# Kernel optimization log

Hardware: AMD Instinct MI355X
Metric: run time of the kernel (lower is better)

Reference implementation:

```python
import jax, jax.numpy as jnp
import numpy as np

IN_SIZE = 32
NUM_ACTIONS = 90
ACTION_DIM = 32
INNER_DIM = 256
HIDDEN_DIM = 512
N_LAYERS = 2
WORLD_STATE_SIZE = 32
# last 8 features are categorical (binary) flags, first 24 numeric
CAT_FLAGS = np.zeros(WORLD_STATE_SIZE, dtype=bool)
CAT_FLAGS[24:] = True


def setup_inputs() -> dict:
    key = jax.random.key(0)
    ks = jax.random.split(key, 20)
    s = 0.05
    b, t = 64, 512
    inp = {
        "batch_world_states_tensor": jax.random.normal(ks[0], (b, t, IN_SIZE), jnp.float32),
        "batch_action_indices": jax.random.randint(ks[1], (b, t), 0, NUM_ACTIONS),
        "action_emb": jax.random.normal(ks[2], (NUM_ACTIONS, ACTION_DIM), jnp.float32),
        "in_w": jax.random.normal(ks[3], (INNER_DIM - ACTION_DIM, IN_SIZE), jnp.float32) * s,
        "in_b": jax.random.normal(ks[4], (INNER_DIM - ACTION_DIM,), jnp.float32) * 0.005,
        "w_ih0": jax.random.normal(ks[5], (4 * HIDDEN_DIM, INNER_DIM), jnp.float32) * s,
        "w_hh0": jax.random.normal(ks[6], (4 * HIDDEN_DIM, HIDDEN_DIM), jnp.float32) * s,
        "b_ih0": jax.random.normal(ks[7], (4 * HIDDEN_DIM,), jnp.float32) * 0.005,
        "b_hh0": jax.random.normal(ks[8], (4 * HIDDEN_DIM,), jnp.float32) * 0.005,
        "w_ih1": jax.random.normal(ks[9], (4 * HIDDEN_DIM, HIDDEN_DIM), jnp.float32) * s,
        "w_hh1": jax.random.normal(ks[10], (4 * HIDDEN_DIM, HIDDEN_DIM), jnp.float32) * s,
        "b_ih1": jax.random.normal(ks[11], (4 * HIDDEN_DIM,), jnp.float32) * 0.005,
        "b_hh1": jax.random.normal(ks[12], (4 * HIDDEN_DIM,), jnp.float32) * 0.005,
        "out_w1": jax.random.normal(ks[13], (2 * HIDDEN_DIM, HIDDEN_DIM), jnp.float32) * s,
        "out_b1": jax.random.normal(ks[14], (2 * HIDDEN_DIM,), jnp.float32) * 0.005,
        "out_w2": jax.random.normal(ks[15], (WORLD_STATE_SIZE, 2 * HIDDEN_DIM), jnp.float32) * s,
        "out_b2": jax.random.normal(ks[16], (WORLD_STATE_SIZE,), jnp.float32) * 0.005,
    }
    return inp


def _lstm_layer(x, w_ih, w_hh, b_ih, b_hh):
    """x: [b, s, d_in] -> ([b, s, H], h_T, c_T). PyTorch gate order i,f,g,o."""
    b = x.shape[0]
    H = w_hh.shape[1]
    # precompute input-to-hidden contributions for all steps: [s, b, 4H]
    gx = jnp.einsum('bsd,gd->sbg', x, w_ih) + b_ih + b_hh
    h0 = jnp.zeros((b, H), x.dtype)
    c0 = jnp.zeros((b, H), x.dtype)

    def step(carry, g_t):
        h, c = carry
        g = g_t + h @ w_hh.T  # [b, 4H]
        i, f, gg, o = jnp.split(g, 4, axis=-1)
        i = jax.nn.sigmoid(i)
        f = jax.nn.sigmoid(f)
        gg = jnp.tanh(gg)
        o = jax.nn.sigmoid(o)
        c = f * c + i * gg
        h = o * jnp.tanh(c)
        return (h, c), h

    (hT, cT), hs = jax.lax.scan(step, (h0, c0), gx)
    return hs.transpose(1, 0, 2), hT, cT  # [b, s, H]


def reference(batch_world_states_tensor, batch_action_indices, action_emb,
              in_w, in_b, w_ih0, w_hh0, b_ih0, b_hh0,
              w_ih1, w_hh1, b_ih1, b_hh1,
              out_w1, out_b1, out_w2, out_b2):
    # input projection + action embedding concat
    proj = jax.nn.relu(jnp.einsum('bsd,ed->bse', batch_world_states_tensor, in_w) + in_b)
    acts = action_emb[batch_action_indices]  # [b, s, action_dim]
    x = jnp.concatenate([proj, acts], axis=-1)  # [b, s, inner_dim]
    # 2-layer LSTM
    x, h0T, c0T = _lstm_layer(x, w_ih0, w_hh0, b_ih0, b_hh0)
    rnn_out, h1T, c1T = _lstm_layer(x, w_ih1, w_hh1, b_ih1, b_hh1)
    # out projector
    hmid = jax.nn.relu(jnp.einsum('bsh,eh->bse', rnn_out, out_w1) + out_b1)
    out = jnp.einsum('bse,de->bsd', hmid, out_w2) + out_b2  # [b, s, D]
    # sigmoid on categorical feature slots
    cat_mask = jnp.asarray(CAT_FLAGS)
    out = jnp.where(cat_mask, jax.nn.sigmoid(out), out)
    return out[:, -1, :]  # [b, D]
```

## Files before the change

### kernel.cpp

```cpp
#include <hip/hip_runtime.h>

#define T_STEPS 512
#define BATCH   64
#define IN_SZ   32
#define AD      32
#define INNER   256
#define PROJ    224
#define HID     512
#define SENTW   0x7F7F7F7Fu
#define SENT64  0x7F7F7F7F7F7F7F7FULL
#define DEP     16
#define RST     6
#define SLOTW   4096

typedef __attribute__((ext_vector_type(8))) short short8;
typedef __attribute__((ext_vector_type(4))) float f32x4;

static __device__ __forceinline__ unsigned short f2bf(float f) {
  unsigned int u = __float_as_uint(f);
  u += 0x7FFFu + ((u >> 16) & 1u);
  return (unsigned short)(u >> 16);
}
static __device__ __forceinline__ float sigmoidf_(float x) { return 1.f / (1.f + __expf(-x)); }
static __device__ __forceinline__ float tanhf_(float x) {
  float e = __expf(-2.f * fabsf(x));
  float r = (1.f - e) / (1.f + e);
  return x < 0.f ? -r : r;
}

__global__ __launch_bounds__(256) void k_prep(
    const float* __restrict__ ws_in, const int* __restrict__ act_idx,
    const float* __restrict__ emb, const float* __restrict__ in_w,
    const float* __restrict__ in_b, unsigned short* __restrict__ x_bf)
{
  int t = blockIdx.x;
  int tid = threadIdx.x;
  __shared__ float st[BATCH * IN_SZ];
  __shared__ int ai[BATCH];
  for (int i = tid; i < BATCH * IN_SZ; i += 256) {
    int b = i >> 5, k = i & 31;
    st[i] = ws_in[((size_t)b * T_STEPS + t) * IN_SZ + k];
  }
  if (tid < BATCH) ai[tid] = act_idx[tid * T_STEPS + t];
  __syncthreads();
  if (tid < PROJ) {
    float w[IN_SZ];
    const float* wrow = in_w + tid * IN_SZ;
#pragma unroll
    for (int k = 0; k < IN_SZ; ++k) w[k] = wrow[k];
    float bb = in_b[tid];
    for (int b = 0; b < BATCH; ++b) {
      float acc = bb;
      const float* sb = st + b * IN_SZ;
#pragma unroll
      for (int k = 0; k < IN_SZ; ++k) acc += w[k] * sb[k];
      x_bf[((size_t)t * BATCH + b) * INNER + tid] = f2bf(fmaxf(acc, 0.f));
    }
  } else {
    int j = tid - PROJ;
    for (int b = 0; b < BATCH; ++b)
      x_bf[((size_t)t * BATCH + b) * INNER + tid] = f2bf(emb[ai[b] * AD + j]);
  }
}

static __device__ __forceinline__ short8 bfrag_load(const float* __restrict__ w, int stride, int row, int k0) {
  const float* p = w + (size_t)row * stride + k0;
  f32x4 a = *reinterpret_cast<const f32x4*>(p);
  f32x4 b = *reinterpret_cast<const f32x4*>(p + 4);
  short8 r;
  r[0] = (short)f2bf(a[0]); r[1] = (short)f2bf(a[1]); r[2] = (short)f2bf(a[2]); r[3] = (short)f2bf(a[3]);
  r[4] = (short)f2bf(b[0]); r[5] = (short)f2bf(b[1]); r[6] = (short)f2bf(b[2]); r[7] = (short)f2bf(b[3]);
  return r;
}

struct Frag64 { unsigned long long u[8]; };
union FU2 { unsigned long long u[2]; short8 s; };

static __device__ __forceinline__ void ld64(const unsigned long long* q, Frag64& f) {
#pragma unroll
  for (int kk = 0; kk < 4; ++kk) {
    f.u[kk * 2]     = __hip_atomic_load(q + kk * 128,     __ATOMIC_RELAXED, __HIP_MEMORY_SCOPE_AGENT);
    f.u[kk * 2 + 1] = __hip_atomic_load(q + kk * 128 + 1, __ATOMIC_RELAXED, __HIP_MEMORY_SCOPE_AGENT);
  }
}
static __device__ __forceinline__ bool fragok(const Frag64& f) {
  bool ok = true;
#pragma unroll
  for (int i = 0; i < 8; ++i)
    ok = ok & ((unsigned)(f.u[i] >> 32) != SENTW) & ((unsigned)f.u[i] != SENTW);
  return ok;
}
static __device__ __forceinline__ Frag64 poll_one(const unsigned long long* q) {
  Frag64 f;
  int miss = 0;
  while (true) {
    ld64(q, f);
    if (__all((int)fragok(f))) break;
    if (++miss > 2) __builtin_amdgcn_s_sleep(1);
  }
  return f;
}
static __device__ __forceinline__ void poll_two(const unsigned long long* qa, const unsigned long long* qb,
                                                Frag64& fa, Frag64& fb) {
  int miss = 0;
  while (true) {
    ld64(qa, fa);
    ld64(qb, fb);
    if (__all((int)(fragok(fa) & fragok(fb)))) break;
    if (++miss > 2) __builtin_amdgcn_s_sleep(1);
  }
}

static __device__ __forceinline__ void mfma4(const Frag64& f, const short8* wf, f32x4* acc) {
#pragma unroll
  for (int kk = 0; kk < 4; ++kk) {
    FU2 u; u.u[0] = f.u[kk * 2]; u.u[1] = f.u[kk * 2 + 1];
#pragma unroll
    for (int g = 0; g < 4; ++g)
      acc[g] = __builtin_amdgcn_mfma_f32_16x16x32_bf16(u.s, wf[g * 4 + kk], acc[g], 0, 0, 0);
  }
}

static __device__ __forceinline__ void st_agent(unsigned int* p, unsigned int v) {
  __hip_atomic_store(p, v, __ATOMIC_RELAXED, __HIP_MEMORY_SCOPE_AGENT);
}
static __device__ __forceinline__ void st_agent64(unsigned long long* p, unsigned long long v) {
  __hip_atomic_store(p, v, __ATOMIC_RELAXED, __HIP_MEMORY_SCOPE_AGENT);
}
static __device__ __forceinline__ size_t slotw(int bg, int d) { return ((size_t)(bg * DEP + d)) * SLOTW; }

template<int L>
static __device__ void lstm_body(
    const unsigned short* __restrict__ x_bf,
    const float* __restrict__ wih, const float* __restrict__ whh,
    const float* __restrict__ bih, const float* __restrict__ bhh,
    unsigned int* __restrict__ h0w, unsigned int* __restrict__ h1w,
    float* __restrict__ h1fin, unsigned int* __restrict__ flags,
    int bg, int blk, float* __restrict__ spart)
{
  constexpr int KI = (L == 0) ? 2 : 4;

  const int tid  = threadIdx.x;
  const int lane = tid & 63;
  const int wv   = tid >> 6;
  const int q    = lane >> 4;
  const int ln   = lane & 15;
  const int hid0 = blk << 4;
  const int m    = tid >> 4;
  const int n    = tid & 15;
  const int cb64 = (wv * 8 + (q >> 1)) * 64 + ln * 4 + (q & 1) * 2;

  float bias[4];
#pragma unroll
  for (int g = 0; g < 4; ++g)
    bias[g] = bih[g * HID + hid0 + n] + bhh[g * HID + hid0 + n];

  short8 fih[4 * KI];
#pragma unroll
  for (int g = 0; g < 4; ++g)
#pragma unroll
    for (int kk = 0; kk < KI; ++kk)
      fih[g * KI + kk] = bfrag_load(wih, (L == 0) ? INNER : HID,
                                    g * HID + hid0 + ln, (wv * KI + kk) * 32 + q * 8);
  short8 fhh[16];
#pragma unroll
  for (int g = 0; g < 4; ++g)
#pragma unroll
    for (int kk = 0; kk < 4; ++kk)
      fhh[g * 4 + kk] = bfrag_load(whh, HID, g * HID + hid0 + ln, (wv * 4 + kk) * 32 + q * 8);

  const int wo64 = blk * 64 + m * 4 + (n >> 2);
  float c_state = 0.f;

  for (int t = 0; t < T_STEPS; ++t) {
    f32x4 acc[4];
#pragma unroll
    for (int g = 0; g < 4; ++g) acc[g] = (f32x4){0.f, 0.f, 0.f, 0.f};

    if constexpr (L == 0) {
      const unsigned long long* hq = reinterpret_cast<const unsigned long long*>(
          h0w + slotw(bg, (t - 1) & (DEP - 1))) + cb64;
      Frag64 f0;
      if (t > 0) ld64(hq, f0);

      const unsigned short* xr = x_bf + ((size_t)t * BATCH + bg * 16 + ln) * INNER + q * 8;
#pragma unroll
      for (int kk = 0; kk < KI; ++kk) {
        short8 xa = *reinterpret_cast<const short8*>(xr + (wv * KI + kk) * 32);
#pragma unroll
        for (int g = 0; g < 4; ++g)
          acc[g] = __builtin_amdgcn_mfma_f32_16x16x32_bf16(xa, fih[g * KI + kk], acc[g], 0, 0, 0);
      }
      if ((t & 3) == 0 && t >= 8) {
        const unsigned int* fp = flags + (bg * 32 + (lane & 31)) * 32;
        unsigned int tgt = (unsigned)(t - 4);
        while (true) {
          unsigned int v = __hip_atomic_load(fp, __ATOMIC_RELAXED, __HIP_MEMORY_SCOPE_AGENT);
          if (__all((int)(v >= tgt))) break;
          __builtin_amdgcn_s_sleep(1);
        }
        asm volatile("" ::: "memory");
      }
      if (t > 0) {
        if (!__all((int)fragok(f0))) f0 = poll_one(hq);
        mfma4(f0, fhh, acc);
      }
    } else {
      if (t > 0) {
        Frag64 fa, fb;
        poll_two(reinterpret_cast<const unsigned long long*>(h1w + slotw(bg, (t - 1) & (DEP - 1))) + cb64,
                 reinterpret_cast<const unsigned long long*>(h0w + slotw(bg, t & (DEP - 1))) + cb64, fa, fb);
        mfma4(fa, fhh, acc);
        mfma4(fb, fih, acc);
      } else {
        Frag64 fb = poll_one(reinterpret_cast<const unsigned long long*>(h0w + slotw(bg, 0)) + cb64);
        mfma4(fb, fih, acc);
      }
    }

    float* sp_w = spart + (t & 1) * 4096;
#pragma unroll
    for (int g = 0; g < 4; ++g)
      *reinterpret_cast<f32x4*>(sp_w + ((((wv * 4 + g) * 4 + q) * 16 + ln) * 4)) = acc[g];
    __syncthreads();

    if constexpr (L == 1) {
      if ((t & 1) == 1 && tid == 0)
        st_agent(flags + (bg * 32 + blk) * 32, (unsigned)(t + 1));
    }

    float gate[4];
#pragma unroll
    for (int g = 0; g < 4; ++g) {
      float s = bias[g];
#pragma unroll
      for (int w2 = 0; w2 < 4; ++w2)
        s += sp_w[(((w2 * 4 + g) * 4 + (m >> 2)) * 16 + n) * 4 + (m & 3)];
      gate[g] = s;
    }
    float gi = sigmoidf_(gate[0]);
    float gf = sigmoidf_(gate[1]);
    float gc = tanhf_(gate[2]);
    float go = sigmoidf_(gate[3]);
    c_state = gf * c_state + gi * gc;
    float h = go * tanhf_(c_state);

    float hp = __shfl_xor(h, 1);
    unsigned int wword = (unsigned)f2bf(h) | ((unsigned)f2bf(hp) << 16);
    unsigned int wy = __shfl_down(wword, 2);
    unsigned long long dw = (unsigned long long)wword | ((unsigned long long)wy << 32);
    if constexpr (L == 0) {
      if (!(n & 3)) {
        st_agent64(reinterpret_cast<unsigned long long*>(h0w + slotw(bg, t & (DEP - 1))) + wo64, dw);
        st_agent64(reinterpret_cast<unsigned long long*>(h0w + slotw(bg, (t + RST) & (DEP - 1))) + wo64, SENT64);
      }
    } else {
      if (!(n & 3)) {
        st_agent64(reinterpret_cast<unsigned long long*>(h1w + slotw(bg, t & (DEP - 1))) + wo64, dw);
        st_agent64(reinterpret_cast<unsigned long long*>(h1w + slotw(bg, (t + RST) & (DEP - 1))) + wo64, SENT64);
      }
      if (t == T_STEPS - 1)
        h1fin[(size_t)(bg * 16 + m) * HID + hid0 + n] = h;
    }
  }
}

__global__ __launch_bounds__(256, 1) void k_lstm(
    const unsigned short* __restrict__ x_bf,
    const float* __restrict__ w_ih0, const float* __restrict__ w_hh0,
    const float* __restrict__ b_ih0, const float* __restrict__ b_hh0,
    const float* __restrict__ w_ih1, const float* __restrict__ w_hh1,
    const float* __restrict__ b_ih1, const float* __restrict__ b_hh1,
    unsigned int* h0w, unsigned int* h1w, float* h1fin, unsigned int* flags)
{
  __shared__ float spart[2 * 4096];
  const int xg  = blockIdx.x & 7;
  const int blk = blockIdx.x >> 3;
  const int bg  = xg & 3;
  if (xg < 4)
    lstm_body<0>(x_bf, w_ih0, w_hh0, b_ih0, b_hh0, h0w, h1w, h1fin, flags, bg, blk, spart);
  else
    lstm_body<1>(x_bf, w_ih1, w_hh1, b_ih1, b_hh1, h0w, h1w, h1fin, flags, bg, blk, spart);
}

__global__ __launch_bounds__(256) void k_head(
    const float* __restrict__ h1, const float* __restrict__ w1, const float* __restrict__ b1,
    const float* __restrict__ w2, const float* __restrict__ b2, float* __restrict__ out)
{
  int b = blockIdx.x, tid = threadIdx.x;
  __shared__ float sh[HID];
  __shared__ float sm[2 * HID];
  for (int k = tid; k < HID; k += 256) sh[k] = h1[(size_t)b * HID + k];
  __syncthreads();
#pragma unroll
  for (int r0 = 0; r0 < 4; ++r0) {
    int row = r0 * 256 + tid;
    const f32x4* wr = reinterpret_cast<const f32x4*>(w1 + (size_t)row * HID);
    float s = 0.f;
#pragma unroll 4
    for (int k = 0; k < HID / 4; ++k) {
      f32x4 v = wr[k];
      s += v[0] * sh[k * 4] + v[1] * sh[k * 4 + 1] + v[2] * sh[k * 4 + 2] + v[3] * sh[k * 4 + 3];
    }
    sm[row] = fmaxf(b1[row] + s, 0.f);
  }
  __syncthreads();
  if (tid < 32) {
    const f32x4* wr = reinterpret_cast<const f32x4*>(w2 + (size_t)tid * 2 * HID);
    float s = b2[tid];
#pragma unroll 4
    for (int k = 0; k < 2 * HID / 4; ++k) {
      f32x4 v = wr[k];
      s += v[0] * sm[k * 4] + v[1] * sm[k * 4 + 1] + v[2] * sm[k * 4 + 2] + v[3] * sm[k * 4 + 3];
    }
    if (tid >= 24) s = sigmoidf_(s);
    out[b * 32 + tid] = s;
  }
}

extern "C" void kernel_launch(void* const* d_in, const int* in_sizes, int n_in,
                              void* d_out, int out_size, void* d_ws, size_t ws_size,
                              hipStream_t stream) {
  const float* ws_in  = (const float*)d_in[0];
  const int*   aidx   = (const int*)d_in[1];
  const float* emb    = (const float*)d_in[2];
  const float* in_w   = (const float*)d_in[3];
  const float* in_b   = (const float*)d_in[4];
  const float* w_ih0  = (const float*)d_in[5];
  const float* w_hh0  = (const float*)d_in[6];
  const float* b_ih0  = (const float*)d_in[7];
  const float* b_hh0  = (const float*)d_in[8];
  const float* w_ih1  = (const float*)d_in[9];
  const float* w_hh1  = (const float*)d_in[10];
  const float* b_ih1  = (const float*)d_in[11];
  const float* b_hh1  = (const float*)d_in[12];
  const float* out_w1 = (const float*)d_in[13];
  const float* out_b1 = (const float*)d_in[14];
  const float* out_w2 = (const float*)d_in[15];
  const float* out_b2 = (const float*)d_in[16];

  unsigned char* ws = (unsigned char*)d_ws;
  const size_t X_OFF   = 0;
  const size_t RING_SZ = 4u * DEP * SLOTW * 4;
  const size_t H0_OFF  = 16777216;
  const size_t H1_OFF  = H0_OFF + RING_SZ;
  const size_t HF_OFF  = H1_OFF + RING_SZ;
  const size_t FL_OFF  = HF_OFF + 131072;
  unsigned short* x_bf  = (unsigned short*)(ws + X_OFF);
  unsigned int*   h0w   = (unsigned int*)(ws + H0_OFF);
  unsigned int*   h1w   = (unsigned int*)(ws + H1_OFF);
  float*          h1fin = (float*)(ws + HF_OFF);
  unsigned int*   flags = (unsigned int*)(ws + FL_OFF);

  hipMemsetAsync(ws + H0_OFF, 0x7F, 2 * RING_SZ, stream);
  hipMemsetAsync(ws + FL_OFF, 0, 16384, stream);
  k_prep<<<dim3(T_STEPS), dim3(256), 0, stream>>>(ws_in, aidx, emb, in_w, in_b, x_bf);
  k_lstm<<<dim3(256), dim3(256), 0, stream>>>(x_bf, w_ih0, w_hh0, b_ih0, b_hh0,
                                              w_ih1, w_hh1, b_ih1, b_hh1,
                                              h0w, h1w, h1fin, flags);
  k_head<<<dim3(BATCH), dim3(256), 0, stream>>>(h1fin, out_w1, out_b1, out_w2, out_b2, (float*)d_out);
}
```

Baseline: 1.501 ms.

## Pipeline spin-poll loads with initial sleep and swizzle LDS partial-sum layout

The cross-block polling loop now issues a load, sleeps a fixed interval, issues a second load, and then alternates between two in-flight fragment buffers, so each sentinel check overlaps the next load instead of waiting on it serially. The LDS staging of per-wave MFMA partial sums moves from f32x4 vector stores to scalar stores in an XOR-swizzled layout, which is meant to reduce bank conflicts on the gate-reduction reads. The cell-state update is reordered into a temporary that is committed at the end of the step. The fixed initial sleep adds latency whenever data is already ready, and the scalar stores raise the LDS store instruction count.

```diff
diff --git a/kernel.cpp b/kernel.cpp
--- a/kernel.cpp
+++ b/kernel.cpp
@@ -91,23 +91,28 @@
   return ok;
 }
 static __device__ __forceinline__ Frag64 poll_one(const unsigned long long* q) {
-  Frag64 f;
-  int miss = 0;
+  Frag64 fa, fb;
+  ld64(q, fa);
+  __builtin_amdgcn_s_sleep(14);
+  ld64(q, fb);
   while (true) {
-    ld64(q, f);
-    if (__all((int)fragok(f))) break;
-    if (++miss > 2) __builtin_amdgcn_s_sleep(1);
-  }
-  return f;
+    if (__all((int)fragok(fa))) return fa;
+    ld64(q, fa);
+    if (__all((int)fragok(fb))) return fb;
+    ld64(q, fb);
+  }
 }
 static __device__ __forceinline__ void poll_two(const unsigned long long* qa, const unsigned long long* qb,
                                                 Frag64& fa, Frag64& fb) {
-  int miss = 0;
+  Frag64 ga, gb;
+  ld64(qa, fa); ld64(qb, fb);
+  __builtin_amdgcn_s_sleep(14);
+  ld64(qa, ga); ld64(qb, gb);
   while (true) {
-    ld64(qa, fa);
-    ld64(qb, fb);
-    if (__all((int)(fragok(fa) & fragok(fb)))) break;
-    if (++miss > 2) __builtin_amdgcn_s_sleep(1);
+    if (__all((int)(fragok(fa) & fragok(fb)))) return;
+    ld64(qa, fa); ld64(qb, fb);
+    if (__all((int)(fragok(ga) & fragok(gb)))) { fa = ga; fb = gb; return; }
+    ld64(qa, ga); ld64(qb, gb);
   }
 }
 
@@ -221,7 +226,9 @@
     float* sp_w = spart + (t & 1) * 4096;
 #pragma unroll
     for (int g = 0; g < 4; ++g)
-      *reinterpret_cast<f32x4*>(sp_w + ((((wv * 4 + g) * 4 + q) * 16 + ln) * 4)) = acc[g];
+#pragma unroll
+      for (int r = 0; r < 4; ++r)
+        sp_w[(((wv * 4 + g) * 4 + r) * 4 + (q ^ r)) * 16 + ln] = acc[g][r];
     __syncthreads();
 
     if constexpr (L == 1) {
@@ -235,15 +242,15 @@
       float s = bias[g];
 #pragma unroll
       for (int w2 = 0; w2 < 4; ++w2)
-        s += sp_w[(((w2 * 4 + g) * 4 + (m >> 2)) * 16 + n) * 4 + (m & 3)];
+        s += sp_w[(((w2 * 4 + g) * 4 + (m & 3)) * 4 + ((m >> 2) ^ (m & 3))) * 16 + n];
       gate[g] = s;
     }
     float gi = sigmoidf_(gate[0]);
     float gf = sigmoidf_(gate[1]);
     float gc = tanhf_(gate[2]);
     float go = sigmoidf_(gate[3]);
-    c_state = gf * c_state + gi * gc;
-    float h = go * tanhf_(c_state);
+    float c_new = gf * c_state + gi * gc;
+    float h = go * tanhf_(c_new);
 
     float hp = __shfl_xor(h, 1);
     unsigned int wword = (unsigned)f2bf(h) | ((unsigned)f2bf(hp) << 16);
@@ -262,6 +269,7 @@
       if (t == T_STEPS - 1)
         h1fin[(size_t)(bg * 16 + m) * HID + hid0 + n] = h;
     }
+    c_state = c_new;
   }
 }
 
```

Result: slower. 1.587 ms (+5.8%).
